# Kernel optimization log

Measured on AMD Instinct MI355X. Metric: run time of the kernel, lower is better.

Reference implementation:

```python
import jax, jax.numpy as jnp
import numpy as np

N_NODES = 200000
N_EDGES = 6400000
F_OUT = 128
N_GRAPHS = 64


def setup_inputs() -> dict:
    key = jax.random.key(0)
    ks = jax.random.split(key, 6)
    x = jax.random.normal(ks[0], (N_NODES, 1), dtype=jnp.float32)
    edge_index = jax.random.randint(ks[1], (2, N_EDGES), 0, N_NODES, dtype=jnp.int64)
    batch = jnp.sort(jax.random.randint(ks[2], (N_NODES,), 0, N_GRAPHS, dtype=jnp.int64))
    edge_weights = jax.random.uniform(ks[3], (N_EDGES,), dtype=jnp.float32)
    W_l = jax.random.normal(ks[4], (F_OUT, 1), dtype=jnp.float32)
    b_l = jnp.zeros((F_OUT,), dtype=jnp.float32)
    W_r = jax.random.normal(ks[5], (F_OUT, 1), dtype=jnp.float32)
    return {"x": x, "edge_index": edge_index, "batch": batch,
            "edge_weights": edge_weights, "W_l": W_l, "b_l": b_l, "W_r": W_r}


def reference(x, edge_index, batch, edge_weights, W_l, b_l, W_r):
    # SAGEConv (mean aggregation, edge-weighted messages as in PyG propagate):
    #   out_i = lin_l( mean_{j in N(i)} w_ij * x_j ) + lin_r(x_i)
    n = x.shape[0]
    src, dst = edge_index[0], edge_index[1]
    msgs = x[src] * edge_weights[:, None]                      # [E, 1] gather
    agg_sum = jax.ops.segment_sum(msgs, dst, num_segments=n)  # [N, 1] scatter-add
    deg = jax.ops.segment_sum(jnp.ones((src.shape[0],), x.dtype), dst, num_segments=n)
    agg = agg_sum / jnp.maximum(deg, 1.0)[:, None]             # mean
    h = agg @ W_l.T + b_l + x @ W_r.T                          # [N, F_OUT]
    # dropout(p=0.2) is identity in eval mode -> omitted
    out = jax.ops.segment_max(h, batch, num_segments=N_GRAPHS)  # global_max_pool
    return out
```

## Files before the change

kernel.cpp:

```cpp
#include <hip/hip_runtime.h>
#include <hip/hip_bf16.h>
#include <float.h>
#include <math.h>

constexpr int NN = 200000;
constexpr int NE = 6400000;
constexpr int FO = 128;
constexpr int NG = 64;

constexpr int NCHUNK = 512;
constexpr int CHUNK  = NE / NCHUNK;
constexpr int C4     = CHUNK / 4;
constexpr int BNODES = 1024;
constexpr int NBUK   = (NN + BNODES - 1) / BNODES;

constexpr float Q_SCALE = 4096.0f;
constexpr float Q_INV   = 1.0f / 4096.0f;

constexpr unsigned ENC_NINF = 0x007FFFFFu;

__device__ __forceinline__ unsigned encf(float f) {
    unsigned u = __float_as_uint(f);
    return (u & 0x80000000u) ? ~u : (u | 0x80000000u);
}
__device__ __forceinline__ float decf(unsigned e) {
    unsigned u = (e & 0x80000000u) ? (e & 0x7FFFFFFFu) : ~e;
    return __uint_as_float(u);
}
__device__ __forceinline__ unsigned short q16(float m) {
    int q = __float2int_rn(m * Q_SCALE) + 32768;
    return (unsigned short)min(max(q, 0), 65535);
}

__global__ __launch_bounds__(1024) void k_hist(const int* __restrict__ ei, unsigned* __restrict__ cnt,
                       unsigned* __restrict__ out_enc,
                       const int* __restrict__ batch, int* __restrict__ start) {
    __shared__ unsigned h[NBUK];
    int c = blockIdx.x, tid = threadIdx.x;
    for (int i = tid; i < NBUK; i += 1024) h[i] = 0u;
    if (c == 0) for (int i = tid; i < NG * FO; i += 1024) out_enc[i] = encf(-INFINITY);
    if (c == 1 && tid <= NG) {
        if (tid == NG) start[tid] = NN;
        else {
            int lo = 0, hi = NN;
            while (lo < hi) { int mid = (lo + hi) >> 1; if (batch[mid] < tid) lo = mid + 1; else hi = mid; }
            start[tid] = lo;
        }
    }
    __syncthreads();
    const int4* d4 = (const int4*)(ei + NE + c * CHUNK);
#pragma unroll
    for (int k = 0; k < 4; ++k) {
        int idx = tid + k * 1024;
        if (idx < C4) {
            int4 v = d4[idx];
            atomicAdd(&h[v.x >> 10], 1u);
            atomicAdd(&h[v.y >> 10], 1u);
            atomicAdd(&h[v.z >> 10], 1u);
            atomicAdd(&h[v.w >> 10], 1u);
        }
    }
    __syncthreads();
    for (int i = tid; i < NBUK; i += 1024) cnt[i * NCHUNK + c] = h[i];
}

__global__ __launch_bounds__(NCHUNK) void k_scanA(unsigned* __restrict__ cnt, unsigned* __restrict__ T) {
    __shared__ unsigned s[NCHUNK];
    int b = blockIdx.x, t = threadIdx.x;
    unsigned v = cnt[b * NCHUNK + t];
    s[t] = v;
    __syncthreads();
    for (int off = 1; off < NCHUNK; off <<= 1) {
        unsigned u = (t >= off) ? s[t - off] : 0u;
        __syncthreads();
        s[t] += u;
        __syncthreads();
    }
    cnt[b * NCHUNK + t] = s[t] - v;
    if (t == NCHUNK - 1) T[b] = s[t];
}

__global__ void k_scanB(const unsigned* __restrict__ T, unsigned* __restrict__ B) {
    __shared__ unsigned s[256];
    int t = threadIdx.x;
    unsigned v = (t < NBUK) ? T[t] : 0u;
    s[t] = v;
    __syncthreads();
    for (int off = 1; off < 256; off <<= 1) {
        unsigned u = (t >= off) ? s[t - off] : 0u;
        __syncthreads();
        s[t] += u;
        __syncthreads();
    }
    if (t < NBUK) B[t] = s[t] - v;
    if (t == 255) B[NBUK] = s[255];
}

__global__ __launch_bounds__(1024) void k_sort2(const int* __restrict__ ei,
                        const float* __restrict__ x, const float* __restrict__ w,
                        const unsigned* __restrict__ cnt,
                        const unsigned* __restrict__ T,
                        const unsigned* __restrict__ B,
                        unsigned* __restrict__ rec,
                        int blo, int bhi, unsigned cap) {
    __shared__ unsigned lincl[256];
    __shared__ unsigned loffs[NBUK];
    __shared__ unsigned gbase[NBUK];
    __shared__ unsigned recbuf[CHUNK];
    int c = blockIdx.x, tid = threadIdx.x;
    int nb = bhi - blo;

    unsigned sz = 0;
    if (tid < nb) {
        int b = blo + tid;
        unsigned pre = cnt[b * NCHUNK + c];
        unsigned nxt = (c + 1 < NCHUNK) ? cnt[b * NCHUNK + c + 1] : T[b];
        sz = nxt - pre;
        gbase[b] = B[b] - B[blo] + pre;
    }
    if (tid < 256) lincl[tid] = sz;
    __syncthreads();
    for (int off = 1; off < 256; off <<= 1) {
        unsigned v = 0;
        if (tid < 256 && tid >= off) v = lincl[tid - off];
        __syncthreads();
        if (tid < 256) lincl[tid] += v;
        __syncthreads();
    }
    if (tid < nb) loffs[blo + tid] = lincl[tid] - sz;
    __syncthreads();

    const int4*   s4 = (const int4*)(ei + c * CHUNK);
    const int4*   d4 = (const int4*)(ei + NE + c * CHUNK);
    const float4* w4 = (const float4*)(w + c * CHUNK);
    const bool t3 = tid < (C4 - 3 * 1024);

    int4 dv0 = d4[tid], dv1 = d4[tid + 1024], dv2 = d4[tid + 2048];
    int4 dv3 = t3 ? d4[tid + 3072] : make_int4(-1, -1, -1, -1);
    int4 sv0 = s4[tid], sv1 = s4[tid + 1024], sv2 = s4[tid + 2048];
    int4 sv3 = t3 ? s4[tid + 3072] : make_int4(0, 0, 0, 0);
    float4 wv0 = w4[tid], wv1 = w4[tid + 1024], wv2 = w4[tid + 2048];
    float4 wv3 = t3 ? w4[tid + 3072] : make_float4(0.f, 0.f, 0.f, 0.f);

    int bb0 = dv0.x >> 10, bb1 = dv0.y >> 10, bb2  = dv0.z >> 10, bb3  = dv0.w >> 10;
    int bb4 = dv1.x >> 10, bb5 = dv1.y >> 10, bb6  = dv1.z >> 10, bb7  = dv1.w >> 10;
    int bb8 = dv2.x >> 10, bb9 = dv2.y >> 10, bb10 = dv2.z >> 10, bb11 = dv2.w >> 10;
    int bb12 = dv3.x >> 10, bb13 = dv3.y >> 10, bb14 = dv3.z >> 10, bb15 = dv3.w >> 10;
    unsigned dl0 = (unsigned)(dv0.x & 1023) << 16, dl1 = (unsigned)(dv0.y & 1023) << 16;
    unsigned dl2 = (unsigned)(dv0.z & 1023) << 16, dl3 = (unsigned)(dv0.w & 1023) << 16;
    unsigned dl4 = (unsigned)(dv1.x & 1023) << 16, dl5 = (unsigned)(dv1.y & 1023) << 16;
    unsigned dl6 = (unsigned)(dv1.z & 1023) << 16, dl7 = (unsigned)(dv1.w & 1023) << 16;
    unsigned dl8 = (unsigned)(dv2.x & 1023) << 16, dl9 = (unsigned)(dv2.y & 1023) << 16;
    unsigned dl10 = (unsigned)(dv2.z & 1023) << 16, dl11 = (unsigned)(dv2.w & 1023) << 16;
    unsigned dl12 = (unsigned)(dv3.x & 1023) << 16, dl13 = (unsigned)(dv3.y & 1023) << 16;
    unsigned dl14 = (unsigned)(dv3.z & 1023) << 16, dl15 = (unsigned)(dv3.w & 1023) << 16;
    const float *p0 = x + sv0.x, *p1 = x + sv0.y, *p2  = x + sv0.z, *p3  = x + sv0.w;
    const float *p4 = x + sv1.x, *p5 = x + sv1.y, *p6  = x + sv1.z, *p7  = x + sv1.w;
    const float *p8 = x + sv2.x, *p9 = x + sv2.y, *p10 = x + sv2.z, *p11 = x + sv2.w;
    const float *p12 = x + sv3.x, *p13 = x + sv3.y, *p14 = x + sv3.z, *p15 = x + sv3.w;

    float g0, g1, g2, g3, g4, g5, g6, g7, g8, g9, g10, g11, g12, g13, g14, g15;
    asm volatile(
        "global_load_dword %0, %8, off\n\t"  "global_load_dword %1, %9, off\n\t"
        "global_load_dword %2, %10, off\n\t" "global_load_dword %3, %11, off\n\t"
        "global_load_dword %4, %12, off\n\t" "global_load_dword %5, %13, off\n\t"
        "global_load_dword %6, %14, off\n\t" "global_load_dword %7, %15, off"
        : "=&v"(g0), "=&v"(g1), "=&v"(g2), "=&v"(g3),
          "=&v"(g4), "=&v"(g5), "=&v"(g6), "=&v"(g7)
        : "v"(p0), "v"(p1), "v"(p2), "v"(p3), "v"(p4), "v"(p5), "v"(p6), "v"(p7));
    asm volatile(
        "global_load_dword %0, %8, off\n\t"  "global_load_dword %1, %9, off\n\t"
        "global_load_dword %2, %10, off\n\t" "global_load_dword %3, %11, off\n\t"
        "global_load_dword %4, %12, off\n\t" "global_load_dword %5, %13, off\n\t"
        "global_load_dword %6, %14, off\n\t" "global_load_dword %7, %15, off"
        : "=&v"(g8), "=&v"(g9), "=&v"(g10), "=&v"(g11),
          "=&v"(g12), "=&v"(g13), "=&v"(g14), "=&v"(g15)
        : "v"(p8), "v"(p9), "v"(p10), "v"(p11), "v"(p12), "v"(p13), "v"(p14), "v"(p15));

    unsigned ls0, ls1, ls2, ls3, ls4, ls5, ls6, ls7;
    unsigned ls8, ls9, ls10, ls11, ls12, ls13, ls14, ls15;
#define RANK(LS, BB) LS = ((BB) >= blo && (BB) < bhi) ? atomicAdd(&loffs[BB], 1u) : 0xFFFFFFFFu;
    RANK(ls0, bb0)   RANK(ls1, bb1)   RANK(ls2, bb2)   RANK(ls3, bb3)
    RANK(ls4, bb4)   RANK(ls5, bb5)   RANK(ls6, bb6)   RANK(ls7, bb7)
    RANK(ls8, bb8)   RANK(ls9, bb9)   RANK(ls10, bb10) RANK(ls11, bb11)
    RANK(ls12, bb12) RANK(ls13, bb13) RANK(ls14, bb14) RANK(ls15, bb15)
#undef RANK

    asm volatile("s_waitcnt vmcnt(0)"
        : "+v"(g0), "+v"(g1), "+v"(g2), "+v"(g3), "+v"(g4), "+v"(g5), "+v"(g6), "+v"(g7),
          "+v"(g8), "+v"(g9), "+v"(g10), "+v"(g11), "+v"(g12), "+v"(g13), "+v"(g14), "+v"(g15)
        :: "memory");
    __builtin_amdgcn_sched_barrier(0);

#define WREC(LS, DL, G, W) if ((LS) != 0xFFFFFFFFu) recbuf[LS] = (DL) | (unsigned)q16((G) * (W));
    WREC(ls0, dl0, g0, wv0.x)    WREC(ls1, dl1, g1, wv0.y)
    WREC(ls2, dl2, g2, wv0.z)    WREC(ls3, dl3, g3, wv0.w)
    WREC(ls4, dl4, g4, wv1.x)    WREC(ls5, dl5, g5, wv1.y)
    WREC(ls6, dl6, g6, wv1.z)    WREC(ls7, dl7, g7, wv1.w)
    WREC(ls8, dl8, g8, wv2.x)    WREC(ls9, dl9, g9, wv2.y)
    WREC(ls10, dl10, g10, wv2.z) WREC(ls11, dl11, g11, wv2.w)
    WREC(ls12, dl12, g12, wv3.x) WREC(ls13, dl13, g13, wv3.y)
    WREC(ls14, dl14, g14, wv3.z) WREC(ls15, dl15, g15, wv3.w)
#undef WREC
    __syncthreads();

    int wave = tid >> 6, lane = tid & 63;
    for (int lb = wave; lb < nb; lb += 16) {
        unsigned s0 = lb ? lincl[lb - 1] : 0u;
        unsigned s1 = lincl[lb];
        unsigned gb = gbase[blo + lb];
        for (unsigned i = s0 + lane; i < s1; i += 64) {
            unsigned g = gb + (i - s0);
            if (g < cap) rec[g] = recbuf[i];
        }
    }
}

__global__ __launch_bounds__(1024) void k_bucket2(const unsigned* __restrict__ rec,
                         const unsigned* __restrict__ B,
                         const float* __restrict__ x,
                         const float* __restrict__ Wl, const float* __restrict__ Wr,
                         const int* __restrict__ start_g,
                         unsigned* __restrict__ out_enc, int blo) {
    __shared__ unsigned long long acc[BNODES];
    __shared__ float2 mx[BNODES];
    __shared__ unsigned gmax[8 * FO];
    __shared__ int st[NG + 1];
    int b = blo + blockIdx.x, tid = threadIdx.x;
    for (int i = tid; i < BNODES; i += 1024) acc[i] = 0ull;
    gmax[tid] = ENC_NINF;
    if (tid <= NG) st[tid] = start_g[tid];
    __syncthreads();

    unsigned b0r = B[blo];
    unsigned r0 = B[b] - b0r, r1 = B[b + 1] - b0r;
    for (unsigned r = r0 + tid; r < r1; r += 1024) {
        unsigned v = rec[r];
        atomicAdd(&acc[v >> 16], (1ull << 48) | (unsigned long long)(v & 0xFFFFu));
    }
    __syncthreads();

    int n0 = b * BNODES;
    for (int i = tid; i < BNODES; i += 1024) {
        int n = n0 + i;
        unsigned long long a = acc[i];
        float cn = (float)(unsigned)(a >> 48);
        float sum = ((float)(a & 0xFFFFFFFFFFFFull) - 32768.0f * cn) * Q_INV;
        mx[i] = make_float2(sum / fmaxf(cn, 1.0f), (n < NN) ? x[n] : 0.f);
    }
    __syncthreads();

    int f = tid & (FO - 1);
    int seg = tid >> 7;
    int i0 = seg * 128;
    float wl = Wl[f], wr = Wr[f];
    int g0; { int lo = 0, hi = NG; while (lo < hi) { int m = (lo + hi + 1) >> 1; if (st[m] <= n0) lo = m; else hi = m - 1; } g0 = lo; }
    int ns = n0 + i0;
    int g;  { int lo = 0, hi = NG; while (lo < hi) { int m = (lo + hi + 1) >> 1; if (st[m] <= ns) lo = m; else hi = m - 1; } g = lo; }
    int nxt = (g < NG) ? st[g + 1] : 0x7FFFFFFF;
    float m = -INFINITY;
#define FLUSH(G, M) if ((M) > -INFINITY) { int sl = (G) - g0; unsigned ev = encf(M); \
        if (sl >= 0 && sl < 8) atomicMax(&gmax[sl * FO + f], ev); \
        else atomicMax(&out_enc[(G) * FO + f], ev); }
    for (int i = i0; i < i0 + 128; ++i) {
        int n = n0 + i;
        if (n >= NN) break;
        while (n >= nxt) { FLUSH(g, m); m = -INFINITY; ++g; nxt = (g < NG) ? st[g + 1] : 0x7FFFFFFF; }
        float2 v = mx[i];
        m = fmaxf(m, fmaf(v.x, wl, v.y * wr));
    }
    FLUSH(g, m)
#undef FLUSH
    __syncthreads();

    { int s = tid >> 7, ff = tid & (FO - 1);
      unsigned v = gmax[s * FO + ff];
      int gg = g0 + s;
      if (v != ENC_NINF && gg < NG) atomicMax(&out_enc[gg * FO + ff], v); }
}

__global__ void k_decode(const unsigned* __restrict__ out_enc,
                         const float* __restrict__ bl, float* __restrict__ out) {
    int i = blockIdx.x * blockDim.x + threadIdx.x;
    if (i >= NG * FO) return;
    out[i] = decf(out_enc[i]) + bl[i & (FO - 1)];
}

constexpr float FP_SCALE = 16777216.0f;
constexpr float FP_INV   = 1.0f / FP_SCALE;
__device__ __forceinline__ unsigned long long pack_msg(float m) {
    return (1ull << 48) + (unsigned long long)(__float2ll_rn(m * FP_SCALE) + (1ll << 30));
}
__global__ void k_init1(unsigned long long* __restrict__ agg, unsigned* __restrict__ out_enc,
                        const int* __restrict__ batch, int* __restrict__ start) {
    int i = blockIdx.x * blockDim.x + threadIdx.x;
    if (i < NN) agg[i] = 0ull;
    if (i < NG * FO) out_enc[i] = encf(-INFINITY);
    if (i <= NG) {
        if (i == NG) start[i] = NN;
        else {
            int lo = 0, hi = NN;
            while (lo < hi) { int mid = (lo + hi) >> 1; if (batch[mid] < i) lo = mid + 1; else hi = mid; }
            start[i] = lo;
        }
    }
}
__global__ void k_scatter1(const int* __restrict__ ei, const float* __restrict__ x,
                           const float* __restrict__ w, unsigned long long* __restrict__ agg) {
    int t = blockIdx.x * blockDim.x + threadIdx.x;
    int e0 = t * 4;
    if (e0 >= NE) return;
    int4 sv = *(const int4*)(ei + e0);
    int4 dv = *(const int4*)(ei + NE + e0);
    float4 wv = *(const float4*)(w + e0);
    atomicAdd(&agg[dv.x], pack_msg(x[sv.x] * wv.x));
    atomicAdd(&agg[dv.y], pack_msg(x[sv.y] * wv.y));
    atomicAdd(&agg[dv.z], pack_msg(x[sv.z] * wv.z));
    atomicAdd(&agg[dv.w], pack_msg(x[sv.w] * wv.w));
}
__global__ void k_max1(const unsigned long long* __restrict__ agg, const float* __restrict__ x,
                       const float* __restrict__ Wl, const float* __restrict__ Wr,
                       const int* __restrict__ start, unsigned* __restrict__ out_enc) {
    int g = blockIdx.x;
    int lo = start[g], hi = start[g + 1];
    if (hi - lo <= 0) return;
    int per = (hi - lo + gridDim.y - 1) / gridDim.y;
    int a0 = lo + blockIdx.y * per, a1 = min(a0 + per, hi);
    if (a0 >= a1) return;
    int f = threadIdx.x;
    float wl = Wl[f], wr = Wr[f], m = -INFINITY;
    for (int i = a0; i < a1; ++i) {
        unsigned long long v = agg[i];
        int cnt = (int)(v >> 48);
        long long sfp = (long long)(v & 0xFFFFFFFFFFFFull) - ((long long)cnt << 30);
        float av = ((float)sfp * FP_INV) / fmaxf((float)cnt, 1.0f);
        m = fmaxf(m, fmaf(av, wl, x[i] * wr));
    }
    atomicMax(&out_enc[g * FO + f], encf(m));
}

extern "C" void kernel_launch(void* const* d_in, const int* in_sizes, int n_in,
                              void* d_out, int out_size, void* d_ws, size_t ws_size,
                              hipStream_t stream) {
    const float* x  = (const float*)d_in[0];
    const int*   ei = (const int*)d_in[1];
    const int*   bt = (const int*)d_in[2];
    const float* ew = (const float*)d_in[3];
    const float* Wl = (const float*)d_in[4];
    const float* bl = (const float*)d_in[5];
    const float* Wr = (const float*)d_in[6];
    float* out = (float*)d_out;
    char* ws = (char*)d_ws;

    const size_t FIXED = (size_t)NBUK * NCHUNK * 4
                       + 1024 + 1024
                       + 32768
                       + 512 + 256;
    int nphase = 0;
    unsigned cap = 0;
    for (int p = 1; p <= 3; ++p) {
        unsigned c = (unsigned)(NE / p) + 16384u;
        if (ws_size >= FIXED + (size_t)c * 4) { nphase = p; cap = c; break; }
    }

    if (nphase) {
        size_t off = 0;
        unsigned* rec  = (unsigned*)(ws + off); off += (size_t)cap * 4;           off = (off + 15) & ~15ull;
        unsigned* cnt  = (unsigned*)(ws + off); off += (size_t)NBUK * NCHUNK * 4; off = (off + 15) & ~15ull;
        unsigned* T    = (unsigned*)(ws + off); off += 1024;
        unsigned* B    = (unsigned*)(ws + off); off += 1024;
        unsigned* out_enc = (unsigned*)(ws + off); off += 32768;
        int*      start   = (int*)(ws + off);

        k_hist<<<NCHUNK, 1024, 0, stream>>>(ei, cnt, out_enc, bt, start);
        k_scanA<<<NBUK, NCHUNK, 0, stream>>>(cnt, T);
        k_scanB<<<1, 256, 0, stream>>>(T, B);
        int per = (NBUK + nphase - 1) / nphase;
        for (int p = 0; p < nphase; ++p) {
            int blo = p * per;
            int bhi = min(blo + per, NBUK);
            if (blo >= bhi) break;
            k_sort2<<<NCHUNK, 1024, 0, stream>>>(ei, x, ew, cnt, T, B, rec, blo, bhi, cap);
            k_bucket2<<<bhi - blo, 1024, 0, stream>>>(rec, B, x, Wl, Wr, start, out_enc, blo);
        }
        k_decode<<<(NG * FO + 255) / 256, 256, 0, stream>>>(out_enc, bl, out);
    } else {
        unsigned long long* agg = (unsigned long long*)ws;
        unsigned* out_enc = (unsigned*)(ws + 1600000);
        int*      start   = (int*)(ws + 1600000 + 32768);
        k_init1<<<(NN + 255) / 256, 256, 0, stream>>>(agg, out_enc, bt, start);
        k_scatter1<<<(NE / 4 + 255) / 256, 256, 0, stream>>>(ei, x, ew, agg);
        k_max1<<<dim3(NG, 32), FO, 0, stream>>>(agg, x, Wl, Wr, start, out_enc);
        k_decode<<<(NG * FO + 255) / 256, 256, 0, stream>>>(out_enc, bl, out);
    }
}
```

Before: 95.96 us.

## Split fused bucket+max kernel into mean-write kernel and separate per-graph max kernel

```diff
diff --git a/kernel.cpp b/kernel.cpp
--- a/kernel.cpp
+++ b/kernel.cpp
@@ -16,8 +16,6 @@
 
 constexpr float Q_SCALE = 4096.0f;
 constexpr float Q_INV   = 1.0f / 4096.0f;
-
-constexpr unsigned ENC_NINF = 0x007FFFFFu;
 
 __device__ __forceinline__ unsigned encf(float f) {
     unsigned u = __float_as_uint(f);
@@ -216,67 +214,55 @@
     }
 }
 
-__global__ __launch_bounds__(1024) void k_bucket2(const unsigned* __restrict__ rec,
+__global__ __launch_bounds__(1024) void k_bucket(const unsigned* __restrict__ rec,
                          const unsigned* __restrict__ B,
-                         const float* __restrict__ x,
-                         const float* __restrict__ Wl, const float* __restrict__ Wr,
-                         const int* __restrict__ start_g,
-                         unsigned* __restrict__ out_enc, int blo) {
+                         float* __restrict__ mean, int blo) {
     __shared__ unsigned long long acc[BNODES];
-    __shared__ float2 mx[BNODES];
-    __shared__ unsigned gmax[8 * FO];
-    __shared__ int st[NG + 1];
     int b = blo + blockIdx.x, tid = threadIdx.x;
     for (int i = tid; i < BNODES; i += 1024) acc[i] = 0ull;
-    gmax[tid] = ENC_NINF;
-    if (tid <= NG) st[tid] = start_g[tid];
-    __syncthreads();
-
-    unsigned b0r = B[blo];
-    unsigned r0 = B[b] - b0r, r1 = B[b + 1] - b0r;
+    __syncthreads();
+    unsigned b0 = B[blo];
+    unsigned r0 = B[b] - b0, r1 = B[b + 1] - b0;
     for (unsigned r = r0 + tid; r < r1; r += 1024) {
         unsigned v = rec[r];
         atomicAdd(&acc[v >> 16], (1ull << 48) | (unsigned long long)(v & 0xFFFFu));
     }
     __syncthreads();
-
     int n0 = b * BNODES;
     for (int i = tid; i < BNODES; i += 1024) {
         int n = n0 + i;
-        unsigned long long a = acc[i];
-        float cn = (float)(unsigned)(a >> 48);
-        float sum = ((float)(a & 0xFFFFFFFFFFFFull) - 32768.0f * cn) * Q_INV;
-        mx[i] = make_float2(sum / fmaxf(cn, 1.0f), (n < NN) ? x[n] : 0.f);
-    }
-    __syncthreads();
-
-    int f = tid & (FO - 1);
-    int seg = tid >> 7;
-    int i0 = seg * 128;
+        if (n < NN) {
+            unsigned long long a = acc[i];
+            float cn = (float)(unsigned)(a >> 48);
+            float sq = (float)(a & 0xFFFFFFFFFFFFull);
+            float sum = (sq - 32768.0f * cn) * Q_INV;
+            mean[n] = sum / fmaxf(cn, 1.0f);
+        }
+    }
+}
+
+constexpr int SPLITS = 16;
+__global__ void k_max8(const float* __restrict__ mean, const float* __restrict__ x,
+                       const float* __restrict__ Wl, const float* __restrict__ Wr,
+                       const int* __restrict__ start, unsigned* __restrict__ out_enc) {
+    int g = blockIdx.x;
+    int lo = start[g], hi = start[g + 1];
+    int len = hi - lo;
+    if (len <= 0) return;
+    int per = (len + gridDim.y - 1) / gridDim.y;
+    int a0 = lo + blockIdx.y * per;
+    int a1 = min(a0 + per, hi);
+    if (a0 >= a1) return;
+    int f = threadIdx.x;
     float wl = Wl[f], wr = Wr[f];
-    int g0; { int lo = 0, hi = NG; while (lo < hi) { int m = (lo + hi + 1) >> 1; if (st[m] <= n0) lo = m; else hi = m - 1; } g0 = lo; }
-    int ns = n0 + i0;
-    int g;  { int lo = 0, hi = NG; while (lo < hi) { int m = (lo + hi + 1) >> 1; if (st[m] <= ns) lo = m; else hi = m - 1; } g = lo; }
-    int nxt = (g < NG) ? st[g + 1] : 0x7FFFFFFF;
-    float m = -INFINITY;
-#define FLUSH(G, M) if ((M) > -INFINITY) { int sl = (G) - g0; unsigned ev = encf(M); \
-        if (sl >= 0 && sl < 8) atomicMax(&gmax[sl * FO + f], ev); \
-        else atomicMax(&out_enc[(G) * FO + f], ev); }
-    for (int i = i0; i < i0 + 128; ++i) {
-        int n = n0 + i;
-        if (n >= NN) break;
-        while (n >= nxt) { FLUSH(g, m); m = -INFINITY; ++g; nxt = (g < NG) ? st[g + 1] : 0x7FFFFFFF; }
-        float2 v = mx[i];
-        m = fmaxf(m, fmaf(v.x, wl, v.y * wr));
-    }
-    FLUSH(g, m)
-#undef FLUSH
-    __syncthreads();
-
-    { int s = tid >> 7, ff = tid & (FO - 1);
-      unsigned v = gmax[s * FO + ff];
-      int gg = g0 + s;
-      if (v != ENC_NINF && gg < NG) atomicMax(&out_enc[gg * FO + ff], v); }
+    float m0 = -INFINITY, m1 = -INFINITY;
+    int i = a0;
+    for (; i + 2 <= a1; i += 2) {
+        m0 = fmaxf(m0, fmaf(mean[i],     wl, x[i]     * wr));
+        m1 = fmaxf(m1, fmaf(mean[i + 1], wl, x[i + 1] * wr));
+    }
+    if (i < a1) m0 = fmaxf(m0, fmaf(mean[i], wl, x[i] * wr));
+    atomicMax(&out_enc[g * FO + f], encf(fmaxf(m0, m1)));
 }
 
 __global__ void k_decode(const unsigned* __restrict__ out_enc,
@@ -354,6 +340,7 @@
 
     const size_t FIXED = (size_t)NBUK * NCHUNK * 4
                        + 1024 + 1024
+                       + 800000
                        + 32768
                        + 512 + 256;
     int nphase = 0;
@@ -369,6 +356,7 @@
         unsigned* cnt  = (unsigned*)(ws + off); off += (size_t)NBUK * NCHUNK * 4; off = (off + 15) & ~15ull;
         unsigned* T    = (unsigned*)(ws + off); off += 1024;
         unsigned* B    = (unsigned*)(ws + off); off += 1024;
+        float*    mean = (float*)(ws + off);    off += 800000;                    off = (off + 15) & ~15ull;
         unsigned* out_enc = (unsigned*)(ws + off); off += 32768;
         int*      start   = (int*)(ws + off);
 
@@ -381,8 +369,9 @@
             int bhi = min(blo + per, NBUK);
             if (blo >= bhi) break;
             k_sort2<<<NCHUNK, 1024, 0, stream>>>(ei, x, ew, cnt, T, B, rec, blo, bhi, cap);
-            k_bucket2<<<bhi - blo, 1024, 0, stream>>>(rec, B, x, Wl, Wr, start, out_enc, blo);
-        }
+            k_bucket<<<bhi - blo, 1024, 0, stream>>>(rec, B, mean, blo);
+        }
+        k_max8<<<dim3(NG, SPLITS), FO, 0, stream>>>(mean, x, Wl, Wr, start, out_enc);
         k_decode<<<(NG * FO + 255) / 256, 256, 0, stream>>>(out_enc, bl, out);
     } else {
         unsigned long long* agg = (unsigned long long*)ws;
```

After: 90.43 us. 1.06x faster.
